# Optimization experiments

Hardware: AMD Instinct MI355X
Metric: run time of the kernel (lower is better)

Reference implementation:

```python
import jax, jax.numpy as jnp
import numpy as np

# Module config (from init_kwargs): Occ3D-nuScenes volume
VOL_MIN = np.array([-40.0, -40.0, -1.0], dtype=np.float32)
VOXEL_SIZE = 0.4
GRID_SHAPE = (200, 200, 16)  # (vol_max - vol_min) / voxel_size
K = 6          # fixed per-gaussian window; covers radii <= 0.6m (bbox span <= 5 voxels)
N_GAUSS = 32768
N_DIMS = 16


def setup_inputs() -> dict:
    key = jax.random.key(0)
    k1, k2, k3, k4, k5 = jax.random.split(key, 5)
    # Means strictly inside the volume with 1m margin so bboxes stay in-grid.
    lo = jnp.array([-39.0, -39.0, 0.0], dtype=jnp.float32)
    hi = jnp.array([39.0, 39.0, 4.4], dtype=jnp.float32)
    means3d = jax.random.uniform(k1, (N_GAUSS, 3), minval=lo, maxval=hi, dtype=jnp.float32)
    # SPD covariances: Q diag(s) Q^T with eigenvalues in [0.01, 0.04]
    A = jax.random.normal(k2, (N_GAUSS, 3, 3), dtype=jnp.float32)
    Q, _ = jnp.linalg.qr(A)
    s = jax.random.uniform(k3, (N_GAUSS, 3), minval=0.01, maxval=0.04, dtype=jnp.float32)
    covs = jnp.einsum('nij,nj,nkj->nik', Q, s, Q)
    opacities = jax.random.uniform(k4, (N_GAUSS,), dtype=jnp.float32)
    features = jax.random.normal(k5, (N_GAUSS, N_DIMS), dtype=jnp.float32)
    return {"means3d": means3d, "covs": covs, "opacities": opacities, "features": features}


def reference(means3d, covs, opacities, features):
    N, D = features.shape
    dim_x, dim_y, dim_z = GRID_SHAPE
    total = dim_x * dim_y * dim_z
    vol_min = jnp.asarray(VOL_MIN)

    inv_covs = jnp.linalg.inv(covs)                                  # [N,3,3]
    radii = 3.0 * jnp.sqrt(jnp.diagonal(covs, axis1=-2, axis2=-1))   # [N,3]

    # Bounding box in voxel indices (trunc toward zero, like the triton .to(int32))
    s = (means3d - radii - vol_min) / VOXEL_SIZE
    e = (means3d + radii - vol_min) / VOXEL_SIZE
    start = jnp.maximum(0, s.astype(jnp.int32))                      # [N,3]
    end = jnp.minimum(jnp.array(GRID_SHAPE, jnp.int32), e.astype(jnp.int32) + 1)

    offs = jnp.arange(K, dtype=jnp.int32)
    ix = start[:, 0:1] + offs   # [N,K]
    iy = start[:, 1:2] + offs
    iz = start[:, 2:3] + offs
    mask = ((ix < end[:, 0:1])[:, :, None, None]
            & (iy < end[:, 1:2])[:, None, :, None]
            & (iz < end[:, 2:3])[:, None, None, :])                  # [N,K,K,K]

    # Voxel-corner minus mean offsets (matches kernel: x*vs + vol_min - m)
    px = ix.astype(means3d.dtype) * VOXEL_SIZE + vol_min[0] - means3d[:, 0:1]  # [N,K]
    py = iy.astype(means3d.dtype) * VOXEL_SIZE + vol_min[1] - means3d[:, 1:2]
    pz = iz.astype(means3d.dtype) * VOXEL_SIZE + vol_min[2] - means3d[:, 2:3]
    d = jnp.stack(jnp.broadcast_arrays(px[:, :, None, None],
                                       py[:, None, :, None],
                                       pz[:, None, None, :]), axis=-1)  # [N,K,K,K,3]

    mahal = jnp.einsum('nxyzi,nij,nxyzj->nxyz', d, inv_covs, d)      # [N,K,K,K]
    density = opacities[:, None, None, None] * jnp.exp(-0.5 * mahal)
    density = jnp.where(mask, density, 0.0)

    flat_idx = (ix[:, :, None, None] * (dim_y * dim_z)
                + iy[:, None, :, None] * dim_z
                + iz[:, None, None, :])                               # [N,K,K,K]
    idx = flat_idx.reshape(-1)

    grid_density = jnp.zeros((total,), density.dtype).at[idx].add(density.reshape(-1))

    contrib = density[..., None] * features[:, None, None, None, :]   # [N,K,K,K,D]
    grid_feats = jnp.zeros((total, D), density.dtype).at[:, -1].set(1e-5)
    grid_feats = grid_feats.at[idx].add(contrib.reshape(-1, D))
    grid_feats = grid_feats / jnp.clip(grid_density, 1e-6, None)[:, None]

    return grid_density.reshape(GRID_SHAPE), grid_feats.reshape(*GRID_SHAPE, D)
```

## Files before the change

### kernel.cpp

```cpp
#include <hip/hip_runtime.h>
#include <math.h>

constexpr int   GX = 200, GY = 200, GZ = 16;
constexpr int   TOTAL = GX * GY * GZ;
constexpr int   ND = 16;
constexpr int   KW = 6;
constexpr float VS = 0.4f;
constexpr float VMINX = -40.0f, VMINY = -40.0f, VMINZ = -1.0f;

constexpr int   TS = 4;
constexpr int   TX = 50, TY = 50, TZ = 4;
constexpr int   NT = TX * TY * TZ;
constexpr int   RS = 20;
constexpr int   CAP = 128;
constexpr int   BR  = 12;
constexpr float NHL2E = -0.72134752044448170f;


__device__ __forceinline__ unsigned bf16_rne(float x) {
    unsigned u = __float_as_uint(x);
    return (u + 0x7fffu + ((u >> 16) & 1u)) >> 16;
}

__global__ __launch_bounds__(64) void gv_rec(
    const float* __restrict__ means, const float* __restrict__ covs,
    const float* __restrict__ opac,  const float* __restrict__ feats,
    float* __restrict__ gdata, int n)
{
    int g = blockIdx.x * 64 + threadIdx.x;
    if (g >= n) return;
    const float* cv = covs + (size_t)g * 9;
    float a = cv[0], b = cv[1], c = cv[2], d = cv[4], e = cv[5], f = cv[8];
    float A = d * f - e * e;
    float B = c * e - b * f;
    float C = b * e - c * d;
    float invdet = 1.0f / (a * A + b * B + c * C);
    float mx = means[g * 3 + 0], my = means[g * 3 + 1], mz = means[g * 3 + 2];
    float rx = 3.0f * sqrtf(a), ry = 3.0f * sqrtf(d), rz = 3.0f * sqrtf(f);
    int sx = max(0, (int)((mx - rx - VMINX) / VS));
    int sy = max(0, (int)((my - ry - VMINY) / VS));
    int sz = max(0, (int)((mz - rz - VMINZ) / VS));
    int ex = min(GX, (int)((mx + rx - VMINX) / VS) + 1); ex = min(ex, sx + KW);
    int ey = min(GY, (int)((my + ry - VMINY) / VS) + 1); ey = min(ey, sy + KW);
    int ez = min(GZ, (int)((mz + rz - VMINZ) / VS) + 1); ez = min(ez, sz + KW);

    float rec[RS];
    rec[0] = mx; rec[1] = my; rec[2] = mz; rec[3] = opac[g];
    rec[4] = (A * invdet) * NHL2E;
    rec[5] = (B * invdet) * (2.0f * NHL2E);
    rec[6] = (C * invdet) * (2.0f * NHL2E);
    rec[7] = ((a * f - c * c) * invdet) * NHL2E;
    rec[8] = ((b * c - a * e) * invdet) * (2.0f * NHL2E);
    rec[9] = ((a * d - b * b) * invdet) * NHL2E;
    rec[10] = __int_as_float(sx | (sy << 8) | (sz << 16));
    rec[11] = __int_as_float(ex | (ey << 8) | (ez << 16));
    const float* fr = feats + (size_t)g * ND;
#pragma unroll
    for (int q = 0; q < 8; ++q) {
        unsigned lo = bf16_rne(fr[2 * q]);
        unsigned hi = bf16_rne(fr[2 * q + 1]);
        rec[12 + q] = __uint_as_float(lo | (hi << 16));
    }
    float4* dst = (float4*)(gdata + (size_t)g * RS);
#pragma unroll
    for (int q = 0; q < 5; ++q) dst[q] = ((const float4*)rec)[q];
}

__global__ __launch_bounds__(256) void gv_bin(
    const float* __restrict__ gdata, int* __restrict__ counts,
    int* __restrict__ entries, int n)
{
    int gid = blockIdx.x * 256 + threadIdx.x;
    int g = gid >> 3;
    if (g >= n) return;
    int c = gid & 7;
    int dx = c & 1, dy = (c >> 1) & 1, dz = (c >> 2) & 1;

    const float2 se = *(const float2*)(gdata + (size_t)g * RS + 10);
    int spk = __float_as_int(se.x), epk = __float_as_int(se.y);
    int sx = spk & 255, sy = (spk >> 8) & 255, sz = (spk >> 16) & 255;
    int ex = epk & 255, ey = (epk >> 8) & 255, ez = (epk >> 16) & 255;

    int tx0 = sx >> 2, nx = ((ex - 1) >> 2) - tx0;
    int ty0 = sy >> 2, ny = ((ey - 1) >> 2) - ty0;
    int tz0 = sz >> 2, nz = ((ez - 1) >> 2) - tz0;

    if (dx <= nx && dy <= ny && dz <= nz) {
        int tile = ((tx0 + dx) * TY + (ty0 + dy)) * TZ + (tz0 + dz);
        int slot = atomicAdd(&counts[tile], 1);
        if (slot < CAP) entries[(size_t)tile * CAP + slot] = g;
    }
}

__global__ __launch_bounds__(256) void gv_tile(
    const float* __restrict__ gdata, const int* __restrict__ counts,
    const int* __restrict__ entries, float* __restrict__ out)
{
    const int wv   = threadIdx.x >> 6;
    const int lane = threadIdx.x & 63;
    const int p    = blockIdx.x * 4 + wv;
    const int tz   = p % TZ;
    const int ty   = (p / TZ) % TY;
    const int tx   = p / (TZ * TY);

    __shared__ float sbuf[4][2][BR * RS];

    const int lz = lane & 3, ly = (lane >> 2) & 3, lx = lane >> 4;
    const int ix = tx * TS + lx, iy = ty * TS + ly, iz = tz * TS + lz;
    const float pxc = (float)ix * VS + VMINX;
    const float pyc = (float)iy * VS + VMINY;
    const float pzc = (float)iz * VS + VMINZ;

    float accd = 0.0f;
    float accf[ND];
#pragma unroll
    for (int c = 0; c < ND; ++c) accf[c] = 0.0f;
    accf[ND - 1] = 1e-5f;

    const int cnt = __builtin_amdgcn_readfirstlane(min(counts[p], CAP));
    const int* __restrict__ el = entries + (size_t)p * CAP;

    const int  rl = lane / 5;
    const int  fc = lane - rl * 5;
    const bool stager = lane < 60;
    const int  wslot = rl * RS + fc * 4;

    if (cnt > 0) {
        const int nb = (cnt + BR - 1) / BR;
        float* b0 = &sbuf[wv][0][0];
        float* b1 = &sbuf[wv][1][0];

        float4 vn; int idn2 = 0;
        if (stager) {
            int id0 = el[min(rl, cnt - 1)];
            float4 v0 = *(const float4*)(gdata + (size_t)id0 * RS + fc * 4);
            *(float4*)(b0 + wslot) = v0;
            int idn = el[min(BR + rl, cnt - 1)];
            vn = *(const float4*)(gdata + (size_t)idn * RS + fc * 4);
            idn2 = el[min(2 * BR + rl, cnt - 1)];
        }

        for (int b = 0; b < nb; ++b) {
            if (b + 1 < nb && stager) {
                float* dstb = ((b + 1) & 1) ? b1 : b0;
                *(float4*)(dstb + wslot) = vn;
                vn = *(const float4*)(gdata + (size_t)idn2 * RS + fc * 4);
                idn2 = el[min((b + 3) * BR + rl, cnt - 1)];
            }
            const float* rb = (b & 1) ? b1 : b0;
            const int rn = min(BR, cnt - b * BR);
            for (int r = 0; r < rn; ++r) {
                const float* rec = rb + r * RS;
                float4 c2 = *(const float4*)(rec + 8);
                int spk = __float_as_int(c2.z), epk = __float_as_int(c2.w);
                int sx = spk & 255, sy = (spk >> 8) & 255, sz = (spk >> 16) & 255;
                int ex = epk & 255, ey = (epk >> 8) & 255, ez = (epk >> 16) & 255;
                bool in = (ix >= sx) & (ix < ex)
                        & (iy >= sy) & (iy < ey)
                        & (iz >= sz) & (iz < ez);

                float4 c0 = *(const float4*)(rec);
                float4 c1 = *(const float4*)(rec + 4);
                float px = pxc - c0.x;
                float py = pyc - c0.y;
                float pz = pzc - c0.z;
                float q = c1.x * px * px + c1.w * py * py + c2.y * pz * pz
                        + c1.y * px * py + c1.z * px * pz + c2.x * py * pz;
                float dens = c0.w * __builtin_amdgcn_exp2f(q);
                dens = in ? dens : 0.0f;
                accd += dens;

                uint4 fA = *(const uint4*)(rec + 12);
                uint4 fB = *(const uint4*)(rec + 16);
#define BFLO(u) __uint_as_float((u) << 16)
#define BFHI(u) __uint_as_float((u) & 0xffff0000u)
                accf[0]  = fmaf(dens, BFLO(fA.x), accf[0]);
                accf[1]  = fmaf(dens, BFHI(fA.x), accf[1]);
                accf[2]  = fmaf(dens, BFLO(fA.y), accf[2]);
                accf[3]  = fmaf(dens, BFHI(fA.y), accf[3]);
                accf[4]  = fmaf(dens, BFLO(fA.z), accf[4]);
                accf[5]  = fmaf(dens, BFHI(fA.z), accf[5]);
                accf[6]  = fmaf(dens, BFLO(fA.w), accf[6]);
                accf[7]  = fmaf(dens, BFHI(fA.w), accf[7]);
                accf[8]  = fmaf(dens, BFLO(fB.x), accf[8]);
                accf[9]  = fmaf(dens, BFHI(fB.x), accf[9]);
                accf[10] = fmaf(dens, BFLO(fB.y), accf[10]);
                accf[11] = fmaf(dens, BFHI(fB.y), accf[11]);
                accf[12] = fmaf(dens, BFLO(fB.z), accf[12]);
                accf[13] = fmaf(dens, BFHI(fB.z), accf[13]);
                accf[14] = fmaf(dens, BFLO(fB.w), accf[14]);
                accf[15] = fmaf(dens, BFHI(fB.w), accf[15]);
#undef BFLO
#undef BFHI
            }
        }
    }

    const int flat = (ix * GY + iy) * GZ + iz;
    out[flat] = accd;
    float inv = 1.0f / fmaxf(accd, 1e-6f);
    float4* fo = (float4*)(out + TOTAL + (size_t)flat * ND);
#pragma unroll
    for (int q = 0; q < 4; ++q) {
        float4 w;
        w.x = accf[q * 4 + 0] * inv;
        w.y = accf[q * 4 + 1] * inv;
        w.z = accf[q * 4 + 2] * inv;
        w.w = accf[q * 4 + 3] * inv;
        fo[q] = w;
    }
}

extern "C" void kernel_launch(void* const* d_in, const int* in_sizes, int n_in,
                              void* d_out, int out_size, void* d_ws, size_t ws_size,
                              hipStream_t stream) {
    const float* means = (const float*)d_in[0];
    const float* covs  = (const float*)d_in[1];
    const float* opac  = (const float*)d_in[2];
    const float* feats = (const float*)d_in[3];
    float* out = (float*)d_out;
    const int n = in_sizes[2];

    float* gdata   = (float*)d_ws;
    int*   counts  = (int*)(gdata + (size_t)n * RS);
    int*   entries = counts + ((NT + 63) & ~63);

    hipMemsetAsync(counts, 0, NT * sizeof(int), stream);
    gv_rec<<<(n + 63) / 64, 64, 0, stream>>>(means, covs, opac, feats, gdata, n);
    gv_bin<<<(n * 8 + 255) / 256, 256, 0, stream>>>(gdata, counts, entries, n);
    gv_tile<<<NT / 4, 256, 0, stream>>>(gdata, counts, entries, out);
}
```

Before: 103.5 us.

## Use 4x4x8 tiles with two z-voxels per lane and packed FMA accumulation

Each wave now covers a 4x4x8 tile, so every lane computes two voxels stacked in z. This halves the tile count and the number of per-gaussian record loads. The xy part of the quadratic form is shared between the two voxels, and the 16 feature accumulators become 2-wide vectors so the compiler can emit packed FMAs. The memset of the tile counters is folded into the record kernel, removing one launch. The cost is more registers per lane, and taller tiles mean more gaussians per tile, which risks hitting CAP=128 and dropping entries.

```diff
diff --git a/kernel.cpp b/kernel.cpp
--- a/kernel.cpp
+++ b/kernel.cpp
@@ -9,13 +9,16 @@
 constexpr float VMINX = -40.0f, VMINY = -40.0f, VMINZ = -1.0f;
 
 constexpr int   TS = 4;
-constexpr int   TX = 50, TY = 50, TZ = 4;
+constexpr int   TSZ = 8;
+constexpr int   TX = 50, TY = 50, TZ = 2;
 constexpr int   NT = TX * TY * TZ;
 constexpr int   RS = 20;
 constexpr int   CAP = 128;
 constexpr int   BR  = 12;
 constexpr float NHL2E = -0.72134752044448170f;
 
+typedef float v2f __attribute__((ext_vector_type(2)));
+
 
 __device__ __forceinline__ unsigned bf16_rne(float x) {
     unsigned u = __float_as_uint(x);
@@ -25,10 +28,11 @@
 __global__ __launch_bounds__(64) void gv_rec(
     const float* __restrict__ means, const float* __restrict__ covs,
     const float* __restrict__ opac,  const float* __restrict__ feats,
-    float* __restrict__ gdata, int n)
+    float* __restrict__ gdata, int* __restrict__ counts, int n)
 {
     int g = blockIdx.x * 64 + threadIdx.x;
     if (g >= n) return;
+    if (g < NT) counts[g] = 0;
     const float* cv = covs + (size_t)g * 9;
     float a = cv[0], b = cv[1], c = cv[2], d = cv[4], e = cv[5], f = cv[8];
     float A = d * f - e * e;
@@ -83,7 +87,7 @@
 
     int tx0 = sx >> 2, nx = ((ex - 1) >> 2) - tx0;
     int ty0 = sy >> 2, ny = ((ey - 1) >> 2) - ty0;
-    int tz0 = sz >> 2, nz = ((ez - 1) >> 2) - tz0;
+    int tz0 = sz >> 3, nz = ((ez - 1) >> 3) - tz0;
 
     if (dx <= nx && dy <= ny && dz <= nz) {
         int tile = ((tx0 + dx) * TY + (ty0 + dy)) * TZ + (tz0 + dz);
@@ -99,23 +103,26 @@
     const int wv   = threadIdx.x >> 6;
     const int lane = threadIdx.x & 63;
     const int p    = blockIdx.x * 4 + wv;
-    const int tz   = p % TZ;
-    const int ty   = (p / TZ) % TY;
-    const int tx   = p / (TZ * TY);
+    const int tz   = p & 1;
+    const int rem  = p >> 1;
+    const int ty   = rem % TY;
+    const int tx   = rem / TY;
 
     __shared__ float sbuf[4][2][BR * RS];
 
     const int lz = lane & 3, ly = (lane >> 2) & 3, lx = lane >> 4;
-    const int ix = tx * TS + lx, iy = ty * TS + ly, iz = tz * TS + lz;
-    const float pxc = (float)ix * VS + VMINX;
-    const float pyc = (float)iy * VS + VMINY;
-    const float pzc = (float)iz * VS + VMINZ;
-
-    float accd = 0.0f;
-    float accf[ND];
-#pragma unroll
-    for (int c = 0; c < ND; ++c) accf[c] = 0.0f;
-    accf[ND - 1] = 1e-5f;
+    const int ix = tx * TS + lx, iy = ty * TS + ly;
+    const int iz0 = tz * TSZ + lz, iz1 = iz0 + 4;
+    const float pxc  = (float)ix  * VS + VMINX;
+    const float pyc  = (float)iy  * VS + VMINY;
+    const float pzc0 = (float)iz0 * VS + VMINZ;
+    const float pzc1 = pzc0 + 4.0f * VS;
+
+    v2f accd2 = {0.0f, 0.0f};
+    v2f accf2[ND];
+#pragma unroll
+    for (int c = 0; c < ND; ++c) accf2[c] = (v2f){0.0f, 0.0f};
+    accf2[ND - 1] = (v2f){1e-5f, 1e-5f};
 
     const int cnt = __builtin_amdgcn_readfirstlane(min(counts[p], CAP));
     const int* __restrict__ el = entries + (size_t)p * CAP;
@@ -155,59 +162,64 @@
                 int spk = __float_as_int(c2.z), epk = __float_as_int(c2.w);
                 int sx = spk & 255, sy = (spk >> 8) & 255, sz = (spk >> 16) & 255;
                 int ex = epk & 255, ey = (epk >> 8) & 255, ez = (epk >> 16) & 255;
-                bool in = (ix >= sx) & (ix < ex)
-                        & (iy >= sy) & (iy < ey)
-                        & (iz >= sz) & (iz < ez);
+                bool inxy = (ix >= sx) & (ix < ex) & (iy >= sy) & (iy < ey);
+                bool in0 = inxy & (iz0 >= sz) & (iz0 < ez);
+                bool in1 = inxy & (iz1 >= sz) & (iz1 < ez);
 
                 float4 c0 = *(const float4*)(rec);
                 float4 c1 = *(const float4*)(rec + 4);
-                float px = pxc - c0.x;
-                float py = pyc - c0.y;
-                float pz = pzc - c0.z;
-                float q = c1.x * px * px + c1.w * py * py + c2.y * pz * pz
-                        + c1.y * px * py + c1.z * px * pz + c2.x * py * pz;
-                float dens = c0.w * __builtin_amdgcn_exp2f(q);
-                dens = in ? dens : 0.0f;
-                accd += dens;
+                float px  = pxc  - c0.x;
+                float py  = pyc  - c0.y;
+                float pz0 = pzc0 - c0.z;
+                float pz1 = pzc1 - c0.z;
+                float u    = fmaf(c1.x, px, c1.y * py);
+                float base = fmaf(c1.w * py, py, px * u);
+                float w    = fmaf(c2.x, py, c1.z * px);
+                float q0   = fmaf(fmaf(c2.y, pz0, w), pz0, base);
+                float q1   = fmaf(fmaf(c2.y, pz1, w), pz1, base);
+                float d0 = c0.w * __builtin_amdgcn_exp2f(q0);
+                float d1 = c0.w * __builtin_amdgcn_exp2f(q1);
+                d0 = in0 ? d0 : 0.0f;
+                d1 = in1 ? d1 : 0.0f;
+                v2f dens2 = {d0, d1};
+                accd2 += dens2;
 
                 uint4 fA = *(const uint4*)(rec + 12);
                 uint4 fB = *(const uint4*)(rec + 16);
 #define BFLO(u) __uint_as_float((u) << 16)
 #define BFHI(u) __uint_as_float((u) & 0xffff0000u)
-                accf[0]  = fmaf(dens, BFLO(fA.x), accf[0]);
-                accf[1]  = fmaf(dens, BFHI(fA.x), accf[1]);
-                accf[2]  = fmaf(dens, BFLO(fA.y), accf[2]);
-                accf[3]  = fmaf(dens, BFHI(fA.y), accf[3]);
-                accf[4]  = fmaf(dens, BFLO(fA.z), accf[4]);
-                accf[5]  = fmaf(dens, BFHI(fA.z), accf[5]);
-                accf[6]  = fmaf(dens, BFLO(fA.w), accf[6]);
-                accf[7]  = fmaf(dens, BFHI(fA.w), accf[7]);
-                accf[8]  = fmaf(dens, BFLO(fB.x), accf[8]);
-                accf[9]  = fmaf(dens, BFHI(fB.x), accf[9]);
-                accf[10] = fmaf(dens, BFLO(fB.y), accf[10]);
-                accf[11] = fmaf(dens, BFHI(fB.y), accf[11]);
-                accf[12] = fmaf(dens, BFLO(fB.z), accf[12]);
-                accf[13] = fmaf(dens, BFHI(fB.z), accf[13]);
-                accf[14] = fmaf(dens, BFLO(fB.w), accf[14]);
-                accf[15] = fmaf(dens, BFHI(fB.w), accf[15]);
+#define ACC2(i, f) { float fv = (f); accf2[i] += dens2 * (v2f){fv, fv}; }
+                ACC2(0,  BFLO(fA.x)); ACC2(1,  BFHI(fA.x));
+                ACC2(2,  BFLO(fA.y)); ACC2(3,  BFHI(fA.y));
+                ACC2(4,  BFLO(fA.z)); ACC2(5,  BFHI(fA.z));
+                ACC2(6,  BFLO(fA.w)); ACC2(7,  BFHI(fA.w));
+                ACC2(8,  BFLO(fB.x)); ACC2(9,  BFHI(fB.x));
+                ACC2(10, BFLO(fB.y)); ACC2(11, BFHI(fB.y));
+                ACC2(12, BFLO(fB.z)); ACC2(13, BFHI(fB.z));
+                ACC2(14, BFLO(fB.w)); ACC2(15, BFHI(fB.w));
+#undef ACC2
 #undef BFLO
 #undef BFHI
             }
         }
     }
 
-    const int flat = (ix * GY + iy) * GZ + iz;
-    out[flat] = accd;
-    float inv = 1.0f / fmaxf(accd, 1e-6f);
-    float4* fo = (float4*)(out + TOTAL + (size_t)flat * ND);
+    const int flat0 = (ix * GY + iy) * GZ + iz0;
+    out[flat0]     = accd2.x;
+    out[flat0 + 4] = accd2.y;
+    float inv0 = 1.0f / fmaxf(accd2.x, 1e-6f);
+    float inv1 = 1.0f / fmaxf(accd2.y, 1e-6f);
+    float4* fo0 = (float4*)(out + TOTAL + (size_t)flat0 * ND);
+    float4* fo1 = (float4*)(out + TOTAL + (size_t)(flat0 + 4) * ND);
 #pragma unroll
     for (int q = 0; q < 4; ++q) {
-        float4 w;
-        w.x = accf[q * 4 + 0] * inv;
-        w.y = accf[q * 4 + 1] * inv;
-        w.z = accf[q * 4 + 2] * inv;
-        w.w = accf[q * 4 + 3] * inv;
-        fo[q] = w;
+        float4 w0, w1;
+        w0.x = accf2[q * 4 + 0].x * inv0;  w1.x = accf2[q * 4 + 0].y * inv1;
+        w0.y = accf2[q * 4 + 1].x * inv0;  w1.y = accf2[q * 4 + 1].y * inv1;
+        w0.z = accf2[q * 4 + 2].x * inv0;  w1.z = accf2[q * 4 + 2].y * inv1;
+        w0.w = accf2[q * 4 + 3].x * inv0;  w1.w = accf2[q * 4 + 3].y * inv1;
+        fo0[q] = w0;
+        fo1[q] = w1;
     }
 }
 
@@ -225,8 +237,8 @@
     int*   counts  = (int*)(gdata + (size_t)n * RS);
     int*   entries = counts + ((NT + 63) & ~63);
 
-    hipMemsetAsync(counts, 0, NT * sizeof(int), stream);
-    gv_rec<<<(n + 63) / 64, 64, 0, stream>>>(means, covs, opac, feats, gdata, n);
+    gv_rec<<<(n + 63) / 64, 64, 0, stream>>>(means, covs, opac, feats,
+                                             gdata, counts, n);
     gv_bin<<<(n * 8 + 255) / 256, 256, 0, stream>>>(gdata, counts, entries, n);
     gv_tile<<<NT / 4, 256, 0, stream>>>(gdata, counts, entries, out);
 }
```

After: 99.91 us, median of 2. -3.5%, faster.
